# Performance work log

Measured on AMD Instinct MI355X. Metric: run time of the kernel, lower is better.

## Reference

```python
import jax, jax.numpy as jnp
import numpy as np

B, T, F = 128, 1024, 128
H, A, L = 128, 128, 7


def setup_inputs() -> dict:
    key = jax.random.key(0)
    ks = jax.random.split(key, 10)
    s = 0.1  # init scale
    return {
        "x": jax.random.normal(ks[0], (B, T, F), dtype=jnp.float32),
        "Wih": jax.random.normal(ks[1], (L, 4 * H, F), dtype=jnp.float32) * s,
        "Whh": jax.random.normal(ks[2], (L, 4 * H, H), dtype=jnp.float32) * s,
        "bih": jax.random.normal(ks[3], (L, 4 * H), dtype=jnp.float32) * s,
        "bhh": jax.random.normal(ks[4], (L, 4 * H), dtype=jnp.float32) * s,
        "Wa": jax.random.normal(ks[5], (A, H), dtype=jnp.float32) * s,
        "ba": jax.random.normal(ks[6], (A,), dtype=jnp.float32) * s,
        "Wf": jax.random.normal(ks[7], (1, H), dtype=jnp.float32) * s,
        "bf": jax.random.normal(ks[8], (1,), dtype=jnp.float32) * s,
    }


def _lstm_layer(x, Wih_l, Whh_l, bih_l, bhh_l):
    # x: [B, T, F_in] -> hidden sequence [B, T, H]; PyTorch gate order i,f,g,o.
    b, t, _ = x.shape
    xg = jnp.einsum('bti,gi->btg', x, Wih_l) + bih_l + bhh_l  # [B, T, 4H]

    def step(carry, xg_t):
        h, c = carry
        z = xg_t + h @ Whh_l.T  # [B, 4H]
        i, f, g, o = jnp.split(z, 4, axis=-1)
        c = jax.nn.sigmoid(f) * c + jax.nn.sigmoid(i) * jnp.tanh(g)
        h = jax.nn.sigmoid(o) * jnp.tanh(c)
        return (h, c), h

    h0 = jnp.zeros((b, H), x.dtype)
    (_, _), hs = jax.lax.scan(step, (h0, h0), jnp.swapaxes(xg, 0, 1))
    return jnp.swapaxes(hs, 0, 1)  # [B, T, H]


def reference(x, Wih, Whh, bih, bhh, Wa, ba, Wf, bf):
    out = x
    for l in range(Wih.shape[0]):  # fixed small layer count
        out = _lstm_layer(out, Wih[l], Whh[l], bih[l], bhh[l])
    # attention: softmax over time of tanh(Linear(out))  -> [B, T, A]
    attn = jax.nn.softmax(jnp.tanh(jnp.einsum('bth,ah->bta', out, Wa) + ba), axis=1)
    applied = jnp.einsum('bta,bth->bah', attn, out)  # bmm(attn^T, out): [B, A, H]
    logits = applied[:, -1, :] @ Wf.T + bf  # last attention head row -> [B, 1]
    return jax.nn.sigmoid(logits)
```

## Files before the change

kernel.cpp:

```cpp
#include <hip/hip_runtime.h>
#include <cstdint>
#include <cstddef>

#define DEV __device__ __forceinline__

typedef __attribute__((ext_vector_type(4))) float    f32x4;
typedef __attribute__((ext_vector_type(4))) _Float16 f16x4;
typedef __attribute__((ext_vector_type(8))) _Float16 f16x8;

static constexpr int B_ = 128, T_ = 1024, F_ = 128, H_ = 128, L_ = 7;
static constexpr int M_ = B_ * T_;

DEV float fexp2(float x){
#if __has_builtin(__builtin_amdgcn_exp2f)
  return __builtin_amdgcn_exp2f(x);
#else
  return exp2f(x);
#endif
}
DEV float frcp(float x){
#if __has_builtin(__builtin_amdgcn_rcpf)
  return __builtin_amdgcn_rcpf(x);
#else
  return 1.0f/x;
#endif
}
DEV float fsig(float x){ return frcp(1.f + fexp2(-1.44269504f*x)); }
DEV float ftanh(float x){
  x = fminf(10.f, fmaxf(-10.f, x));
  float e = fexp2(2.88539008f*x);
  return (e - 1.f) * frcp(e + 1.f);
}
DEV f16x4 ntld4(const _Float16* p){ return __builtin_nontemporal_load((const f16x4*)p); }
DEV void  ntst4(_Float16* p, f16x4 v){ __builtin_nontemporal_store(v, (f16x4*)p); }
DEV f16x8 ntld8(const _Float16* p){ return __builtin_nontemporal_load((const f16x8*)p); }

__global__ void k_cvt_x(const float4* __restrict__ x4, f16x4* __restrict__ xo, int n4){
  int i = blockIdx.x*blockDim.x + threadIdx.x;
  int stride = gridDim.x*blockDim.x;
  for (; i < n4; i += stride){
    float4 v = x4[i];
    f16x4 o = {(_Float16)v.x, (_Float16)v.y, (_Float16)v.z, (_Float16)v.w};
    xo[i] = o;
  }
}

__global__ void k_cvt_w(const float* __restrict__ Wih, const float* __restrict__ Whh,
                        const float* __restrict__ bih, const float* __restrict__ bhh,
                        _Float16* __restrict__ Wc, float* __restrict__ biasp){
  int idx = blockIdx.x*blockDim.x + threadIdx.x;
  int l    = idx >> 17;
  int rem  = idx & 131071;
  int m    = rem >> 8;
  int k    = rem & 255;
  int gate = m & 3, hrow = m >> 2;
  int srow = l*512 + gate*128 + hrow;
  float v = (k < 128) ? Whh[(size_t)srow*128 + k] : Wih[(size_t)srow*128 + (k-128)];
  Wc[idx] = (_Float16)v;
  if (idx < L_*512){
    int bl = idx >> 9, r = idx & 511;
    int bh = r >> 2, bg = r & 3;
    int s = bl*512 + bg*128 + bh;
    biasp[idx] = bih[s] + bhh[s];
  }
}

__global__ __launch_bounds__(512, 2) void k_recur(
    const _Float16* __restrict__ xcvt,
    _Float16* __restrict__ buf0, _Float16* __restrict__ buf1,
    const _Float16* __restrict__ Wc, const float4* __restrict__ biasp,
    int* __restrict__ flags){
  const int wg = blockIdx.x;
  const int layer = wg >> 3;
  const int g = wg & 7;
  const int tid = threadIdx.x;
  const int w = tid >> 6, l64 = tid & 63;
  const int q = l64 >> 4, i = l64 & 15;

  const _Float16* src = (layer == 0) ? xcvt : (((layer - 1) & 1) ? buf1 : buf0);
  _Float16* dst = (layer & 1) ? buf1 : buf0;

  __shared__ _Float16 hx[2][16][264];

  f16x8 wf[4][8];
  {
    const _Float16* wbase = Wc + ((size_t)layer*512 + i)*256 + 8*q;
#pragma unroll
    for (int mt = 0; mt < 4; ++mt)
#pragma unroll
      for (int kt = 0; kt < 8; ++kt)
        wf[mt][kt] = *(const f16x8*)(wbase + (size_t)(16*(4*w+mt))*256 + 32*kt);
  }
  f32x4 bs[4];
#pragma unroll
  for (int mt = 0; mt < 4; ++mt){
    float4 bv = biasp[layer*128 + 4*(4*w+mt) + q];
    f32x4 t = {bv.x, bv.y, bv.z, bv.w};
    bs[mt] = t;
  }
  float cst[4] = {0.f, 0.f, 0.f, 0.f};

  const int bb = tid >> 5;
  const int cc = tid & 31;
  const size_t srow = ((size_t)(g*16 + bb))*T_*H_;
  const _Float16* xsrc = src + srow + cc*4;
  _Float16*       hdst = dst + srow + cc*4;
  int* fIn  = flags + ((layer - 1)*8 + g)*128;
  int* fOut = flags + (layer*8 + g)*128;

  auto poll = [&](int* p){
    if (tid == 0){
      while (__hip_atomic_load(p, __ATOMIC_RELAXED, __HIP_MEMORY_SCOPE_AGENT) == 0)
        __builtin_amdgcn_s_sleep(2);
    }
    __syncthreads();
  };

  if (layer > 0) poll(fIn + 0);
  {
    f16x4 z4 = {(_Float16)0.f, (_Float16)0.f, (_Float16)0.f, (_Float16)0.f};
    *(f16x4*)&hx[0][bb][cc*4] = z4;
    f16x4 x0 = ntld4(xsrc);
    *(f16x4*)&hx[0][bb][128 + cc*4] = x0;
  }
  f16x4 xn1 = ntld4(xsrc + (size_t)H_);
  __syncthreads();

  for (int t = 0; t < T_; ++t){
    const int cur = t & 1, nxt = cur ^ 1;
    if (layer > 0 && ((t + 2) & 7) == 0 && (t + 2) < T_) poll(fIn + ((t + 2) >> 3));
    int tp = (t + 2 < T_) ? t + 2 : T_ - 1;
    f16x4 xn2 = ntld4(xsrc + (size_t)tp*H_);
    f16x4 freg;
    if (t > 0) freg = *(const f16x4*)&hx[cur][bb][cc*4];
    f16x8 bf[8];
#pragma unroll
    for (int kt = 0; kt < 8; ++kt)
      bf[kt] = *(const f16x8*)&hx[cur][i][32*kt + 8*q];
    f32x4 acc[4];
#pragma unroll
    for (int mt = 0; mt < 4; ++mt){
      acc[mt] = bs[mt];
#pragma unroll
      for (int kt = 0; kt < 8; ++kt)
        acc[mt] = __builtin_amdgcn_mfma_f32_16x16x32_f16(wf[mt][kt], bf[kt], acc[mt], 0, 0, 0);
    }
    if (t > 0) ntst4(hdst + (size_t)(t - 1)*H_, freg);
#pragma unroll
    for (int mt = 0; mt < 4; ++mt){
      f32x4 z = acc[mt];
      cst[mt] = fsig(z[1])*cst[mt] + fsig(z[0])*ftanh(z[2]);
      float h = fsig(z[3])*ftanh(cst[mt]);
      hx[nxt][i][4*(4*w + mt) + q] = (_Float16)h;
    }
    *(f16x4*)&hx[nxt][bb][128 + cc*4] = xn1;
    xn1 = xn2;
    asm volatile("s_waitcnt lgkmcnt(0)\n\ts_barrier" ::: "memory");
    if (layer < 6 && t > 0 && (t & 7) == 0){
      asm volatile("s_waitcnt vmcnt(0)" ::: "memory");
      __syncthreads();
      if (tid == 0)
        (void)__hip_atomic_fetch_add(fOut + ((t >> 3) - 1), 1, __ATOMIC_RELAXED, __HIP_MEMORY_SCOPE_AGENT);
    }
  }
  {
    f16x4 freg = *(const f16x4*)&hx[0][bb][cc*4];
    ntst4(hdst + (size_t)(T_ - 1)*H_, freg);
  }
  if (layer < 6){
    asm volatile("s_waitcnt vmcnt(0)" ::: "memory");
    __syncthreads();
    if (tid == 0)
      (void)__hip_atomic_fetch_add(fOut + 127, 1, __ATOMIC_RELAXED, __HIP_MEMORY_SCOPE_AGENT);
  }
}

__global__ __launch_bounds__(256) void k_attn(const _Float16* __restrict__ out,
                                              const float* __restrict__ Wa, const float* __restrict__ ba,
                                              const float* __restrict__ Wf, const float* __restrict__ bfv,
                                              float* __restrict__ y){
  int b = blockIdx.x, tid = threadIdx.x;
  __shared__ float was[H_];
  __shared__ float p[T_];
  __shared__ float red[64];
  __shared__ float app[256];
  if (tid < H_) was[tid] = Wa[127*H_ + tid];
  __syncthreads();
  float bav = ba[127];
  for (int t = tid; t < T_; t += 256){
    const _Float16* row = out + (size_t)(b*T_ + t)*H_;
    float acc = 0.f;
#pragma unroll
    for (int k = 0; k < H_; k += 8){
      f16x8 u = ntld8(row + k);
      acc += (float)u[0]*was[k+0] + (float)u[1]*was[k+1]
           + (float)u[2]*was[k+2] + (float)u[3]*was[k+3]
           + (float)u[4]*was[k+4] + (float)u[5]*was[k+5]
           + (float)u[6]*was[k+6] + (float)u[7]*was[k+7];
    }
    p[t] = ftanh(acc + bav);
  }
  __syncthreads();
  float m = -1e30f;
  for (int t = tid; t < T_; t += 256) m = fmaxf(m, p[t]);
  for (int off = 32; off; off >>= 1) m = fmaxf(m, __shfl_xor(m, off));
  if ((tid & 63) == 0) red[tid >> 6] = m;
  __syncthreads();
  if (tid == 0) red[8] = fmaxf(fmaxf(red[0], red[1]), fmaxf(red[2], red[3]));
  __syncthreads();
  float smax = red[8];
  float lsum = 0.f;
  for (int t = tid; t < T_; t += 256){
    float e = fexp2(1.44269504f*(p[t] - smax));
    p[t] = e; lsum += e;
  }
  for (int off = 32; off; off >>= 1) lsum += __shfl_xor(lsum, off);
  if ((tid & 63) == 0) red[16 + (tid >> 6)] = lsum;
  __syncthreads();
  float rden = frcp(red[16] + red[17] + red[18] + red[19]);
  int h = tid & (H_ - 1);
  int half = tid >> 7;
  float acc = 0.f;
  for (int t = half*512; t < half*512 + 512; ++t)
    acc += p[t] * (float)__builtin_nontemporal_load(out + (size_t)(b*T_ + t)*H_ + h);
  app[tid] = acc;
  __syncthreads();
  if (tid < H_){
    float applied = (app[tid] + app[tid + H_]) * rden;
    float v = applied * Wf[tid];
    for (int off = 32; off; off >>= 1) v += __shfl_xor(v, off);
    if (tid == 0)  red[32] = v;
    if (tid == 64) red[33] = v;
  }
  __syncthreads();
  if (tid == 0) y[b] = fsig(red[32] + red[33] + bfv[0]);
}

extern "C" void kernel_launch(void* const* d_in, const int* in_sizes, int n_in,
                              void* d_out, int out_size, void* d_ws, size_t ws_size,
                              hipStream_t stream){
  const float* x   = (const float*)d_in[0];
  const float* Wih = (const float*)d_in[1];
  const float* Whh = (const float*)d_in[2];
  const float* bih = (const float*)d_in[3];
  const float* bhh = (const float*)d_in[4];
  const float* Wa  = (const float*)d_in[5];
  const float* ba  = (const float*)d_in[6];
  const float* Wf  = (const float*)d_in[7];
  const float* bfv = (const float*)d_in[8];
  float* y = (float*)d_out;

  char* ws = (char*)d_ws;
  size_t off = 0;
  auto alloc = [&](size_t bytes) -> void* {
    void* p = ws + off; off += (bytes + 255) & ~(size_t)255; return p;
  };
  _Float16* xcvt  = (_Float16*)alloc((size_t)M_*H_*2);
  _Float16* buf0  = (_Float16*)alloc((size_t)M_*H_*2);
  _Float16* buf1  = (_Float16*)alloc((size_t)M_*H_*2);
  _Float16* Wc    = (_Float16*)alloc((size_t)L_*512*256*2);
  float*    biasp = (float*)   alloc((size_t)L_*512*4);
  int*      flags = (int*)     alloc((size_t)6*8*128*4);

  hipMemsetAsync(flags, 0, (size_t)6*8*128*4, stream);
  k_cvt_x<<<2048, 256, 0, stream>>>((const float4*)x, (f16x4*)xcvt, M_*F_/4);
  k_cvt_w<<<3584, 256, 0, stream>>>(Wih, Whh, bih, bhh, Wc, biasp);
  k_recur<<<56, 512, 0, stream>>>(xcvt, buf0, buf1, Wc, (const float4*)biasp, flags);
  k_attn<<<128, 256, 0, stream>>>(buf0, Wa, ba, Wf, bfv, y);
}
```

Baseline: 1.543 ms.

## Split LSTM recurrence across 16 waves with direct-register input operands

The recurrent kernel moves from 8 to 16 waves per workgroup (1024 threads), so each wave holds two gate tiles instead of four and the per-step MFMA chain is half as long. The input-projection operands now come straight from global memory into registers one step ahead, which shrinks the shared h/x buffer to the hidden state only. The weight and bias layout is permuted to match, the loop is unrolled by two, tanh is rewritten in sigmoid form, and the layer flags become plain stores. In exchange it adds more per-step barrier participants and fewer registers per thread, and it depends on the new global loads arriving in time.

```diff
diff --git a/kernel.cpp b/kernel.cpp
--- a/kernel.cpp
+++ b/kernel.cpp
@@ -5,11 +5,13 @@
 #define DEV __device__ __forceinline__
 
 typedef __attribute__((ext_vector_type(4))) float    f32x4;
+typedef __attribute__((ext_vector_type(2))) _Float16 f16x2;
 typedef __attribute__((ext_vector_type(4))) _Float16 f16x4;
 typedef __attribute__((ext_vector_type(8))) _Float16 f16x8;
 
 static constexpr int B_ = 128, T_ = 1024, F_ = 128, H_ = 128, L_ = 7;
 static constexpr int M_ = B_ * T_;
+static constexpr int NCH = 128;
 
 DEV float fexp2(float x){
 #if __has_builtin(__builtin_amdgcn_exp2f)
@@ -26,12 +28,7 @@
 #endif
 }
 DEV float fsig(float x){ return frcp(1.f + fexp2(-1.44269504f*x)); }
-DEV float ftanh(float x){
-  x = fminf(10.f, fmaxf(-10.f, x));
-  float e = fexp2(2.88539008f*x);
-  return (e - 1.f) * frcp(e + 1.f);
-}
-DEV f16x4 ntld4(const _Float16* p){ return __builtin_nontemporal_load((const f16x4*)p); }
+DEV float ftanh(float x){ return 2.f*frcp(1.f + fexp2(-2.88539008f*x)) - 1.f; }
 DEV void  ntst4(_Float16* p, f16x4 v){ __builtin_nontemporal_store(v, (f16x4*)p); }
 DEV f16x8 ntld8(const _Float16* p){ return __builtin_nontemporal_load((const f16x8*)p); }
 
@@ -47,66 +44,70 @@
 
 __global__ void k_cvt_w(const float* __restrict__ Wih, const float* __restrict__ Whh,
                         const float* __restrict__ bih, const float* __restrict__ bhh,
-                        _Float16* __restrict__ Wc, float* __restrict__ biasp){
+                        _Float16* __restrict__ Wc, float* __restrict__ biasc){
   int idx = blockIdx.x*blockDim.x + threadIdx.x;
   int l    = idx >> 17;
   int rem  = idx & 131071;
-  int m    = rem >> 8;
+  int m2   = rem >> 8;
   int k    = rem & 255;
-  int gate = m & 3, hrow = m >> 2;
-  int srow = l*512 + gate*128 + hrow;
+  int W  = m2 >> 5;
+  int mt = (m2 >> 4) & 1;
+  int q  = (m2 >> 2) & 3;
+  int r  = m2 & 3;
+  int hrow = 8*W + 2*q + mt;
+  int srow = l*512 + r*128 + hrow;
   float v = (k < 128) ? Whh[(size_t)srow*128 + k] : Wih[(size_t)srow*128 + (k-128)];
   Wc[idx] = (_Float16)v;
   if (idx < L_*512){
-    int bl = idx >> 9, r = idx & 511;
-    int bh = r >> 2, bg = r & 3;
-    int s = bl*512 + bg*128 + bh;
-    biasp[idx] = bih[s] + bhh[s];
-  }
-}
-
-__global__ __launch_bounds__(512, 2) void k_recur(
+    int bl = idx >> 9, bm = idx & 511;
+    int bW = bm >> 5, bmt = (bm >> 4) & 1, bq = (bm >> 2) & 3, br = bm & 3;
+    int bs = bl*512 + br*128 + (8*bW + 2*bq + bmt);
+    biasc[idx] = bih[bs] + bhh[bs];
+  }
+}
+
+__global__ __launch_bounds__(1024) void k_wave(
     const _Float16* __restrict__ xcvt,
     _Float16* __restrict__ buf0, _Float16* __restrict__ buf1,
-    const _Float16* __restrict__ Wc, const float4* __restrict__ biasp,
+    const _Float16* __restrict__ Wc, const float4* __restrict__ biasc,
     int* __restrict__ flags){
   const int wg = blockIdx.x;
   const int layer = wg >> 3;
   const int g = wg & 7;
   const int tid = threadIdx.x;
-  const int w = tid >> 6, l64 = tid & 63;
-  const int q = l64 >> 4, i = l64 & 15;
+  const int W = tid >> 6;
+  const int q = (tid >> 4) & 3;
+  const int i = tid & 15;
 
   const _Float16* src = (layer == 0) ? xcvt : (((layer - 1) & 1) ? buf1 : buf0);
   _Float16* dst = (layer & 1) ? buf1 : buf0;
 
-  __shared__ _Float16 hx[2][16][264];
-
-  f16x8 wf[4][8];
+  __shared__ _Float16 hx[2][16][132];
+
+  f16x8 wf[2][8];
   {
-    const _Float16* wbase = Wc + ((size_t)layer*512 + i)*256 + 8*q;
+    const _Float16* wbase = Wc + ((size_t)(layer*512) + 32*W + i)*256 + 8*q;
 #pragma unroll
-    for (int mt = 0; mt < 4; ++mt)
+    for (int mt = 0; mt < 2; ++mt)
 #pragma unroll
       for (int kt = 0; kt < 8; ++kt)
-        wf[mt][kt] = *(const f16x8*)(wbase + (size_t)(16*(4*w+mt))*256 + 32*kt);
-  }
-  f32x4 bs[4];
-#pragma unroll
-  for (int mt = 0; mt < 4; ++mt){
-    float4 bv = biasp[layer*128 + 4*(4*w+mt) + q];
-    f32x4 t = {bv.x, bv.y, bv.z, bv.w};
-    bs[mt] = t;
-  }
-  float cst[4] = {0.f, 0.f, 0.f, 0.f};
-
+        wf[mt][kt] = *(const f16x8*)(wbase + (size_t)(16*mt)*256 + 32*kt);
+  }
+  f32x4 bias0, bias1;
+  {
+    float4 b0 = biasc[layer*128 + 8*W + q];
+    float4 b1 = biasc[layer*128 + 8*W + 4 + q];
+    bias0 = f32x4{b0.x, b0.y, b0.z, b0.w};
+    bias1 = f32x4{b1.x, b1.y, b1.z, b1.w};
+  }
+  float c0 = 0.f, c1 = 0.f;
+
+  const _Float16* xbase = src + ((size_t)(g*16 + i))*T_*H_ + 8*q;
   const int bb = tid >> 5;
   const int cc = tid & 31;
-  const size_t srow = ((size_t)(g*16 + bb))*T_*H_;
-  const _Float16* xsrc = src + srow + cc*4;
-  _Float16*       hdst = dst + srow + cc*4;
-  int* fIn  = flags + ((layer - 1)*8 + g)*128;
-  int* fOut = flags + (layer*8 + g)*128;
+  _Float16* hdst = dst + ((size_t)(g*16 + (bb & 15)))*T_*H_ + cc*4;
+  int* fIn  = flags + ((layer > 0 ? layer - 1 : 0)*8 + g)*NCH;
+  int* fOut = flags + (layer*8 + g)*NCH;
 
   auto poll = [&](int* p){
     if (tid == 0){
@@ -117,53 +118,74 @@
   };
 
   if (layer > 0) poll(fIn + 0);
-  {
+  if (tid < 512){
     f16x4 z4 = {(_Float16)0.f, (_Float16)0.f, (_Float16)0.f, (_Float16)0.f};
     *(f16x4*)&hx[0][bb][cc*4] = z4;
-    f16x4 x0 = ntld4(xsrc);
-    *(f16x4*)&hx[0][bb][128 + cc*4] = x0;
-  }
-  f16x4 xn1 = ntld4(xsrc + (size_t)H_);
-  __syncthreads();
-
-  for (int t = 0; t < T_; ++t){
-    const int cur = t & 1, nxt = cur ^ 1;
-    if (layer > 0 && ((t + 2) & 7) == 0 && (t + 2) < T_) poll(fIn + ((t + 2) >> 3));
-    int tp = (t + 2 < T_) ? t + 2 : T_ - 1;
-    f16x4 xn2 = ntld4(xsrc + (size_t)tp*H_);
-    f16x4 freg;
-    if (t > 0) freg = *(const f16x4*)&hx[cur][bb][cc*4];
-    f16x8 bf[8];
-#pragma unroll
-    for (int kt = 0; kt < 8; ++kt)
-      bf[kt] = *(const f16x8*)&hx[cur][i][32*kt + 8*q];
-    f32x4 acc[4];
-#pragma unroll
-    for (int mt = 0; mt < 4; ++mt){
-      acc[mt] = bs[mt];
-#pragma unroll
-      for (int kt = 0; kt < 8; ++kt)
-        acc[mt] = __builtin_amdgcn_mfma_f32_16x16x32_f16(wf[mt][kt], bf[kt], acc[mt], 0, 0, 0);
-    }
-    if (t > 0) ntst4(hdst + (size_t)(t - 1)*H_, freg);
-#pragma unroll
-    for (int mt = 0; mt < 4; ++mt){
-      f32x4 z = acc[mt];
-      cst[mt] = fsig(z[1])*cst[mt] + fsig(z[0])*ftanh(z[2]);
-      float h = fsig(z[3])*ftanh(cst[mt]);
-      hx[nxt][i][4*(4*w + mt) + q] = (_Float16)h;
-    }
-    *(f16x4*)&hx[nxt][bb][128 + cc*4] = xn1;
-    xn1 = xn2;
-    asm volatile("s_waitcnt lgkmcnt(0)\n\ts_barrier" ::: "memory");
+  }
+  f16x8 bx0 = *(const f16x8*)(xbase +  0);
+  f16x8 bx1 = *(const f16x8*)(xbase + 32);
+  f16x8 bx2 = *(const f16x8*)(xbase + 64);
+  f16x8 bx3 = *(const f16x8*)(xbase + 96);
+  __syncthreads();
+
+#define MF(Wf, Bf, Acc) Acc = __builtin_amdgcn_mfma_f32_16x16x32_f16(Wf, Bf, Acc, 0, 0, 0)
+
+#define BODY(CUR, TT)                                                            \
+  {                                                                              \
+    f16x4 freg = {};                                                             \
+    if ((TT) > 0 && tid < 512) freg = *(const f16x4*)&hx[CUR][bb][cc*4];         \
+    f32x4 a0 = bias0, a1 = bias1;                                                \
+                           \
+    MF(wf[0][4], bx0, a0); MF(wf[1][4], bx0, a1);                                \
+    MF(wf[0][5], bx1, a0); MF(wf[1][5], bx1, a1);                                \
+    MF(wf[0][6], bx2, a0); MF(wf[1][6], bx2, a1);                                \
+    MF(wf[0][7], bx3, a0); MF(wf[1][7], bx3, a1);                                \
+                                                         \
+    f16x8 bf0 = *(const f16x8*)&hx[CUR][i][ 0 + 8*q];                            \
+    f16x8 bf1 = *(const f16x8*)&hx[CUR][i][32 + 8*q];                            \
+    f16x8 bf2 = *(const f16x8*)&hx[CUR][i][64 + 8*q];                            \
+    f16x8 bf3 = *(const f16x8*)&hx[CUR][i][96 + 8*q];                            \
+         \
+    { int rp = (TT) + 1; if (rp > T_ - 1) rp = T_ - 1;                           \
+      const _Float16* xr = xbase + (size_t)rp*H_;                                \
+      bx0 = *(const f16x8*)(xr +  0);                                            \
+      bx1 = *(const f16x8*)(xr + 32);                                            \
+      bx2 = *(const f16x8*)(xr + 64);                                            \
+      bx3 = *(const f16x8*)(xr + 96); }                                          \
+                                                                     \
+    MF(wf[0][0], bf0, a0); MF(wf[1][0], bf0, a1);                                \
+    MF(wf[0][1], bf1, a0); MF(wf[1][1], bf1, a1);                                \
+    MF(wf[0][2], bf2, a0); MF(wf[1][2], bf2, a1);                                \
+    MF(wf[0][3], bf3, a0); MF(wf[1][3], bf3, a1);                                \
+    if ((TT) > 0 && tid < 512) ntst4(hdst + (size_t)((TT) - 1)*H_, freg);        \
+                           \
+    float h0, h1;                                                                \
+    { float si = fsig(a0[0]), sf = fsig(a0[1]);                                  \
+      float gt = ftanh(a0[2]), so = fsig(a0[3]);                                 \
+      c0 = sf*c0 + si*gt; h0 = so*ftanh(c0); }                                   \
+    { float si = fsig(a1[0]), sf = fsig(a1[1]);                                  \
+      float gt = ftanh(a1[2]), so = fsig(a1[3]);                                 \
+      c1 = sf*c1 + si*gt; h1 = so*ftanh(c1); }                                   \
+    f16x2 hv = {(_Float16)h0, (_Float16)h1};                                     \
+    *(f16x2*)&hx[(CUR) ^ 1][i][8*W + 2*q] = hv;                                  \
+    asm volatile("s_waitcnt lgkmcnt(0)\n\ts_barrier" ::: "memory");              \
+  }
+
+  for (int t = 0; t < T_; t += 2){
+    BODY(0, t)
     if (layer < 6 && t > 0 && (t & 7) == 0){
       asm volatile("s_waitcnt vmcnt(0)" ::: "memory");
       __syncthreads();
       if (tid == 0)
-        (void)__hip_atomic_fetch_add(fOut + ((t >> 3) - 1), 1, __ATOMIC_RELAXED, __HIP_MEMORY_SCOPE_AGENT);
+        __hip_atomic_store(fOut + ((t >> 3) - 1), 1, __ATOMIC_RELAXED, __HIP_MEMORY_SCOPE_AGENT);
     }
-  }
-  {
+    if (layer > 0 && ((t + 2) & 7) == 0 && (t + 2) < T_) poll(fIn + ((t + 2) >> 3));
+    BODY(1, t + 1)
+  }
+#undef BODY
+#undef MF
+
+  if (tid < 512){
     f16x4 freg = *(const f16x4*)&hx[0][bb][cc*4];
     ntst4(hdst + (size_t)(T_ - 1)*H_, freg);
   }
@@ -171,7 +193,7 @@
     asm volatile("s_waitcnt vmcnt(0)" ::: "memory");
     __syncthreads();
     if (tid == 0)
-      (void)__hip_atomic_fetch_add(fOut + 127, 1, __ATOMIC_RELAXED, __HIP_MEMORY_SCOPE_AGENT);
+      __hip_atomic_store(fOut + (NCH - 1), 1, __ATOMIC_RELAXED, __HIP_MEMORY_SCOPE_AGENT);
   }
 }
 
@@ -259,12 +281,12 @@
   _Float16* buf0  = (_Float16*)alloc((size_t)M_*H_*2);
   _Float16* buf1  = (_Float16*)alloc((size_t)M_*H_*2);
   _Float16* Wc    = (_Float16*)alloc((size_t)L_*512*256*2);
-  float*    biasp = (float*)   alloc((size_t)L_*512*4);
-  int*      flags = (int*)     alloc((size_t)6*8*128*4);
-
-  hipMemsetAsync(flags, 0, (size_t)6*8*128*4, stream);
+  float*    biasc = (float*)   alloc((size_t)L_*512*4);
+  int*      flags = (int*)     alloc((size_t)L_*8*NCH*4);
+
+  hipMemsetAsync(flags, 0, (size_t)L_*8*NCH*4, stream);
   k_cvt_x<<<2048, 256, 0, stream>>>((const float4*)x, (f16x4*)xcvt, M_*F_/4);
-  k_cvt_w<<<3584, 256, 0, stream>>>(Wih, Whh, bih, bhh, Wc, biasp);
-  k_recur<<<56, 512, 0, stream>>>(xcvt, buf0, buf1, Wc, (const float4*)biasp, flags);
+  k_cvt_w<<<3584, 256, 0, stream>>>(Wih, Whh, bih, bhh, Wc, biasc);
+  k_wave<<<56, 1024, 0, stream>>>(xcvt, buf0, buf1, Wc, (const float4*)biasc, flags);
   k_attn<<<128, 256, 0, stream>>>(buf0, Wa, ba, Wf, bfv, y);
 }
```

After: 2.347 ms. +52.1%, slower.

## Split input projection into producer workgroups feeding recurrent workgroups via ring buffer

Applied to the files above, without the earlier changes.

Adds 56 producer workgroups that compute the input-to-hidden gate projections for 8-timestep chunks into a ring buffer in global memory, with flag-based handshakes. The recurrent workgroups then run only the hidden-to-hidden MFMAs (K=128 instead of 256) and load precomputed gates ahead of time, which halves the serial critical-path matrix work. It also simplifies tanh, unrolls the timestep loop by two, and relaxes the launch bound. The cost is extra global traffic, more flag polling, and the risk that producer throughput or the ring-buffer backpressure becomes the new bottleneck.

```diff
diff --git a/kernel.cpp b/kernel.cpp
--- a/kernel.cpp
+++ b/kernel.cpp
@@ -10,6 +10,9 @@
 
 static constexpr int B_ = 128, T_ = 1024, F_ = 128, H_ = 128, L_ = 7;
 static constexpr int M_ = B_ * T_;
+static constexpr int NCH  = 128;
+static constexpr int RING = 8;
+static constexpr int ROWE = 128*16*4;
 
 DEV float fexp2(float x){
 #if __has_builtin(__builtin_amdgcn_exp2f)
@@ -26,14 +29,18 @@
 #endif
 }
 DEV float fsig(float x){ return frcp(1.f + fexp2(-1.44269504f*x)); }
-DEV float ftanh(float x){
-  x = fminf(10.f, fmaxf(-10.f, x));
-  float e = fexp2(2.88539008f*x);
-  return (e - 1.f) * frcp(e + 1.f);
-}
+DEV float ftanh(float x){ return 2.f*frcp(1.f + fexp2(-2.88539008f*x)) - 1.f; }
+DEV void  ntst4(_Float16* p, f16x4 v){ __builtin_nontemporal_store(v, (f16x4*)p); }
 DEV f16x4 ntld4(const _Float16* p){ return __builtin_nontemporal_load((const f16x4*)p); }
-DEV void  ntst4(_Float16* p, f16x4 v){ __builtin_nontemporal_store(v, (f16x4*)p); }
 DEV f16x8 ntld8(const _Float16* p){ return __builtin_nontemporal_load((const f16x8*)p); }
+
+DEV void poll_flag(int* p, int tid){
+  if (tid == 0){
+    while (__hip_atomic_load(p, __ATOMIC_RELAXED, __HIP_MEMORY_SCOPE_AGENT) == 0)
+      __builtin_amdgcn_s_sleep(2);
+  }
+  __syncthreads();
+}
 
 __global__ void k_cvt_x(const float4* __restrict__ x4, f16x4* __restrict__ xo, int n4){
   int i = blockIdx.x*blockDim.x + threadIdx.x;
@@ -47,133 +54,204 @@
 
 __global__ void k_cvt_w(const float* __restrict__ Wih, const float* __restrict__ Whh,
                         const float* __restrict__ bih, const float* __restrict__ bhh,
-                        _Float16* __restrict__ Wc, float* __restrict__ biasp){
+                        _Float16* __restrict__ WhhC, _Float16* __restrict__ WihC,
+                        float* __restrict__ biasc){
   int idx = blockIdx.x*blockDim.x + threadIdx.x;
-  int l    = idx >> 17;
-  int rem  = idx & 131071;
-  int m    = rem >> 8;
-  int k    = rem & 255;
-  int gate = m & 3, hrow = m >> 2;
-  int srow = l*512 + gate*128 + hrow;
-  float v = (k < 128) ? Whh[(size_t)srow*128 + k] : Wih[(size_t)srow*128 + (k-128)];
-  Wc[idx] = (_Float16)v;
+  int l   = idx >> 16;
+  int rem = idx & 65535;
+  int m2  = rem >> 7;
+  int k   = rem & 127;
+  int W = m2 >> 6, mt = (m2 >> 4) & 3, q = (m2 >> 2) & 3, r = m2 & 3;
+  int hrow = 16*W + 4*q + mt;
+  int srow = l*512 + r*128 + hrow;
+  WhhC[idx] = (_Float16)Whh[(size_t)srow*128 + k];
+  WihC[idx] = (_Float16)Wih[(size_t)srow*128 + k];
   if (idx < L_*512){
-    int bl = idx >> 9, r = idx & 511;
-    int bh = r >> 2, bg = r & 3;
-    int s = bl*512 + bg*128 + bh;
-    biasp[idx] = bih[s] + bhh[s];
-  }
-}
-
-__global__ __launch_bounds__(512, 2) void k_recur(
+    int bl = idx >> 9, bm = idx & 511;
+    int bW = bm >> 6, bmt = (bm >> 4) & 3, bq = (bm >> 2) & 3, br = bm & 3;
+    int bs = bl*512 + br*128 + (16*bW + 4*bq + bmt);
+    biasc[idx] = bih[bs] + bhh[bs];
+  }
+}
+
+#define MF(Wf, Bf, Acc) Acc = __builtin_amdgcn_mfma_f32_16x16x32_f16(Wf, Bf, Acc, 0, 0, 0)
+
+__global__ __launch_bounds__(512) void k_fused(
     const _Float16* __restrict__ xcvt,
     _Float16* __restrict__ buf0, _Float16* __restrict__ buf1,
-    const _Float16* __restrict__ Wc, const float4* __restrict__ biasp,
-    int* __restrict__ flags){
-  const int wg = blockIdx.x;
-  const int layer = wg >> 3;
-  const int g = wg & 7;
+    const _Float16* __restrict__ WhhC, const _Float16* __restrict__ WihC,
+    const float4* __restrict__ biascF4,
+    _Float16* __restrict__ xz, int* __restrict__ flags){
+  const int wg  = blockIdx.x;
   const int tid = threadIdx.x;
-  const int w = tid >> 6, l64 = tid & 63;
-  const int q = l64 >> 4, i = l64 & 15;
-
-  const _Float16* src = (layer == 0) ? xcvt : (((layer - 1) & 1) ? buf1 : buf0);
-  _Float16* dst = (layer & 1) ? buf1 : buf0;
-
-  __shared__ _Float16 hx[2][16][264];
-
-  f16x8 wf[4][8];
-  {
-    const _Float16* wbase = Wc + ((size_t)layer*512 + i)*256 + 8*q;
-#pragma unroll
-    for (int mt = 0; mt < 4; ++mt)
-#pragma unroll
-      for (int kt = 0; kt < 8; ++kt)
-        wf[mt][kt] = *(const f16x8*)(wbase + (size_t)(16*(4*w+mt))*256 + 32*kt);
-  }
-  f32x4 bs[4];
-#pragma unroll
-  for (int mt = 0; mt < 4; ++mt){
-    float4 bv = biasp[layer*128 + 4*(4*w+mt) + q];
-    f32x4 t = {bv.x, bv.y, bv.z, bv.w};
-    bs[mt] = t;
-  }
-  float cst[4] = {0.f, 0.f, 0.f, 0.f};
-
-  const int bb = tid >> 5;
-  const int cc = tid & 31;
-  const size_t srow = ((size_t)(g*16 + bb))*T_*H_;
-  const _Float16* xsrc = src + srow + cc*4;
-  _Float16*       hdst = dst + srow + cc*4;
-  int* fIn  = flags + ((layer - 1)*8 + g)*128;
-  int* fOut = flags + (layer*8 + g)*128;
-
-  auto poll = [&](int* p){
-    if (tid == 0){
-      while (__hip_atomic_load(p, __ATOMIC_RELAXED, __HIP_MEMORY_SCOPE_AGENT) == 0)
-        __builtin_amdgcn_s_sleep(2);
+  const int W  = tid >> 6;
+  const int lq = (tid >> 4) & 3;
+  const int li = tid & 15;
+
+  __shared__ _Float16 smem[128*132];
+
+  int* recF = flags;
+  int* xzF  = flags + 7*8*NCH;
+
+  if (wg < 56){
+    const int layer = wg >> 3, g = wg & 7;
+    _Float16* dst = (layer & 1) ? buf1 : buf0;
+    _Float16 (*hx)[16][132] = (_Float16(*)[16][132])smem;
+
+    f16x8 wfH[4][4];
+    {
+      const _Float16* wb = WhhC + ((size_t)(layer*512) + 64*W + li)*128 + 8*lq;
+#pragma unroll
+      for (int mt = 0; mt < 4; ++mt)
+#pragma unroll
+        for (int kt = 0; kt < 4; ++kt)
+          wfH[mt][kt] = *(const f16x8*)(wb + (size_t)(16*mt)*128 + 32*kt);
+    }
+    float c0_ = 0.f, c1_ = 0.f, c2_ = 0.f, c3_ = 0.f;
+
+    const int bb = tid >> 5, cc = tid & 31;
+    _Float16* hdst = dst + ((size_t)(g*16 + bb))*T_*H_ + cc*4;
+    const _Float16* xzg = xz + ((size_t)(layer*8 + g))*RING*8*ROWE;
+    int* xzFl = xzF + (layer*8 + g)*NCH;
+    int* myF  = recF + (layer*8 + g)*NCH;
+    const int xzoff = ((16*W + 4*lq)*16 + li)*4;
+
+    poll_flag(xzFl + 0, tid);
+    {
+      f16x4 z4 = {(_Float16)0.f, (_Float16)0.f, (_Float16)0.f, (_Float16)0.f};
+      *(f16x4*)&hx[0][bb][cc*4] = z4;
+    }
+    f16x4 xzA[4], xzB[4];
+#pragma unroll
+    for (int mt = 0; mt < 4; ++mt){
+      xzA[mt] = ntld4(xzg + xzoff + mt*64);
+      xzB[mt] = ntld4(xzg + (size_t)ROWE + xzoff + mt*64);
     }
     __syncthreads();
-  };
-
-  if (layer > 0) poll(fIn + 0);
-  {
-    f16x4 z4 = {(_Float16)0.f, (_Float16)0.f, (_Float16)0.f, (_Float16)0.f};
-    *(f16x4*)&hx[0][bb][cc*4] = z4;
-    f16x4 x0 = ntld4(xsrc);
-    *(f16x4*)&hx[0][bb][128 + cc*4] = x0;
-  }
-  f16x4 xn1 = ntld4(xsrc + (size_t)H_);
-  __syncthreads();
-
-  for (int t = 0; t < T_; ++t){
-    const int cur = t & 1, nxt = cur ^ 1;
-    if (layer > 0 && ((t + 2) & 7) == 0 && (t + 2) < T_) poll(fIn + ((t + 2) >> 3));
-    int tp = (t + 2 < T_) ? t + 2 : T_ - 1;
-    f16x4 xn2 = ntld4(xsrc + (size_t)tp*H_);
-    f16x4 freg;
-    if (t > 0) freg = *(const f16x4*)&hx[cur][bb][cc*4];
-    f16x8 bf[8];
-#pragma unroll
-    for (int kt = 0; kt < 8; ++kt)
-      bf[kt] = *(const f16x8*)&hx[cur][i][32*kt + 8*q];
-    f32x4 acc[4];
-#pragma unroll
-    for (int mt = 0; mt < 4; ++mt){
-      acc[mt] = bs[mt];
-#pragma unroll
-      for (int kt = 0; kt < 8; ++kt)
-        acc[mt] = __builtin_amdgcn_mfma_f32_16x16x32_f16(wf[mt][kt], bf[kt], acc[mt], 0, 0, 0);
-    }
-    if (t > 0) ntst4(hdst + (size_t)(t - 1)*H_, freg);
-#pragma unroll
-    for (int mt = 0; mt < 4; ++mt){
-      f32x4 z = acc[mt];
-      cst[mt] = fsig(z[1])*cst[mt] + fsig(z[0])*ftanh(z[2]);
-      float h = fsig(z[3])*ftanh(cst[mt]);
-      hx[nxt][i][4*(4*w + mt) + q] = (_Float16)h;
-    }
-    *(f16x4*)&hx[nxt][bb][128 + cc*4] = xn1;
-    xn1 = xn2;
-    asm volatile("s_waitcnt lgkmcnt(0)\n\ts_barrier" ::: "memory");
-    if (layer < 6 && t > 0 && (t & 7) == 0){
+
+#define RBODY(CUR, TT, XZ)                                                      \
+  {                                                                             \
+    f16x4 freg = {};                                                            \
+    if ((TT) > 0) freg = *(const f16x4*)&hx[CUR][bb][cc*4];                     \
+    f32x4 a0 = {(float)XZ[0][0], (float)XZ[0][1], (float)XZ[0][2], (float)XZ[0][3]}; \
+    f32x4 a1 = {(float)XZ[1][0], (float)XZ[1][1], (float)XZ[1][2], (float)XZ[1][3]}; \
+    f32x4 a2 = {(float)XZ[2][0], (float)XZ[2][1], (float)XZ[2][2], (float)XZ[2][3]}; \
+    f32x4 a3 = {(float)XZ[3][0], (float)XZ[3][1], (float)XZ[3][2], (float)XZ[3][3]}; \
+    f16x8 bf0 = *(const f16x8*)&hx[CUR][li][ 0 + 8*lq];                         \
+    f16x8 bf1 = *(const f16x8*)&hx[CUR][li][32 + 8*lq];                         \
+    f16x8 bf2 = *(const f16x8*)&hx[CUR][li][64 + 8*lq];                         \
+    f16x8 bf3 = *(const f16x8*)&hx[CUR][li][96 + 8*lq];                         \
+    { int rp = (TT) + 2; if (rp > T_ - 1) rp = T_ - 1;                          \
+      const _Float16* xr = xzg + (size_t)(rp & 63)*ROWE + xzoff;                \
+      XZ[0] = ntld4(xr); XZ[1] = ntld4(xr + 64);                                \
+      XZ[2] = ntld4(xr + 128); XZ[3] = ntld4(xr + 192); }                       \
+    MF(wfH[0][0], bf0, a0); MF(wfH[1][0], bf0, a1);                             \
+    MF(wfH[2][0], bf0, a2); MF(wfH[3][0], bf0, a3);                             \
+    MF(wfH[0][1], bf1, a0); MF(wfH[1][1], bf1, a1);                             \
+    MF(wfH[2][1], bf1, a2); MF(wfH[3][1], bf1, a3);                             \
+    MF(wfH[0][2], bf2, a0); MF(wfH[1][2], bf2, a1);                             \
+    MF(wfH[2][2], bf2, a2); MF(wfH[3][2], bf2, a3);                             \
+    MF(wfH[0][3], bf3, a0); MF(wfH[1][3], bf3, a1);                             \
+    MF(wfH[2][3], bf3, a2); MF(wfH[3][3], bf3, a3);                             \
+    if ((TT) > 0) ntst4(hdst + (size_t)((TT) - 1)*H_, freg);                    \
+    f16x4 hv;                                                                   \
+    { float si = fsig(a0[0]), sf = fsig(a0[1]);                                 \
+      float gt = ftanh(a0[2]), so = fsig(a0[3]);                                \
+      c0_ = sf*c0_ + si*gt; hv[0] = (_Float16)(so*ftanh(c0_)); }                \
+    { float si = fsig(a1[0]), sf = fsig(a1[1]);                                 \
+      float gt = ftanh(a1[2]), so = fsig(a1[3]);                                \
+      c1_ = sf*c1_ + si*gt; hv[1] = (_Float16)(so*ftanh(c1_)); }                \
+    { float si = fsig(a2[0]), sf = fsig(a2[1]);                                 \
+      float gt = ftanh(a2[2]), so = fsig(a2[3]);                                \
+      c2_ = sf*c2_ + si*gt; hv[2] = (_Float16)(so*ftanh(c2_)); }                \
+    { float si = fsig(a3[0]), sf = fsig(a3[1]);                                 \
+      float gt = ftanh(a3[2]), so = fsig(a3[3]);                                \
+      c3_ = sf*c3_ + si*gt; hv[3] = (_Float16)(so*ftanh(c3_)); }                \
+    *(f16x4*)&hx[(CUR) ^ 1][li][16*W + 4*lq] = hv;                              \
+    asm volatile("s_waitcnt lgkmcnt(0)\n\ts_barrier" ::: "memory");             \
+  }
+
+    for (int t = 0; t < T_; t += 2){
+      if ((t & 7) == 6) poll_flag(xzFl + ((t + 2) >> 3), tid);
+      RBODY(0, t, xzA)
+      if (t > 0 && (t & 7) == 0){
+        asm volatile("s_waitcnt vmcnt(0)" ::: "memory");
+        __syncthreads();
+        if (tid == 0)
+          __hip_atomic_store(myF + ((t >> 3) - 1), 1, __ATOMIC_RELAXED, __HIP_MEMORY_SCOPE_AGENT);
+      }
+      RBODY(1, t + 1, xzB)
+    }
+#undef RBODY
+    {
+      f16x4 freg = *(const f16x4*)&hx[0][bb][cc*4];
+      ntst4(hdst + (size_t)(T_ - 1)*H_, freg);
+    }
+    asm volatile("s_waitcnt vmcnt(0)" ::: "memory");
+    __syncthreads();
+    if (tid == 0)
+      __hip_atomic_store(myF + (NCH - 1), 1, __ATOMIC_RELAXED, __HIP_MEMORY_SCOPE_AGENT);
+
+  } else {
+    const int wg2 = wg - 56;
+    const int layer = wg2 >> 3, g = wg2 & 7;
+    const _Float16* hsrc = (layer == 0) ? xcvt : (((layer - 1) & 1) ? buf1 : buf0);
+    _Float16 (*hb)[132] = (_Float16(*)[132])smem;
+    _Float16* xzw = xz + ((size_t)(layer*8 + g))*RING*8*ROWE;
+    int* xzFl = xzF + (layer*8 + g)*NCH;
+    int* inF  = recF + ((layer > 0 ? layer - 1 : 0)*8 + g)*NCH;
+    int* selfF = recF + (layer*8 + g)*NCH;
+
+    const int n  = tid >> 2;
+    const int qd = tid & 3;
+    const int st = n >> 4, sb = n & 15;
+    const _Float16* srcp = hsrc + ((size_t)(g*16 + sb))*T_*H_ + (size_t)st*H_ + qd*32;
+
+    for (int c = 0; c < NCH; ++c){
+      if (layer > 0) poll_flag(inF + c, tid);
+      if (c >= RING) poll_flag(selfF + (c - RING), tid);
+      {
+        const _Float16* sp = srcp + (size_t)(8*c)*H_;
+        f16x8 v0 = ntld8(sp), v1 = ntld8(sp + 8), v2 = ntld8(sp + 16), v3 = ntld8(sp + 24);
+        *(f16x8*)&hb[n][qd*32 +  0] = v0;
+        *(f16x8*)&hb[n][qd*32 +  8] = v1;
+        *(f16x8*)&hb[n][qd*32 + 16] = v2;
+        *(f16x8*)&hb[n][qd*32 + 24] = v3;
+      }
+      __syncthreads();
+#pragma unroll
+      for (int j = 0; j < 4; ++j){
+        const int m0 = 64*W + 16*j;
+        f16x8 A0, A1, A2, A3;
+        {
+          const _Float16* ab = WihC + ((size_t)(layer*512 + m0 + li))*128 + 8*lq;
+          A0 = *(const f16x8*)(ab);      A1 = *(const f16x8*)(ab + 32);
+          A2 = *(const f16x8*)(ab + 64); A3 = *(const f16x8*)(ab + 96);
+        }
+        float4 bv = biascF4[layer*128 + 16*W + 4*j + lq];
+        f32x4 bias = {bv.x, bv.y, bv.z, bv.w};
+        const int hrow = 16*W + 4*lq + j;
+#pragma unroll
+        for (int nt = 0; nt < 8; ++nt){
+          f16x8 B0 = *(const f16x8*)&hb[nt*16 + li][ 0 + 8*lq];
+          f16x8 B1 = *(const f16x8*)&hb[nt*16 + li][32 + 8*lq];
+          f16x8 B2 = *(const f16x8*)&hb[nt*16 + li][64 + 8*lq];
+          f16x8 B3 = *(const f16x8*)&hb[nt*16 + li][96 + 8*lq];
+          f32x4 acc = bias;
+          MF(A0, B0, acc); MF(A1, B1, acc); MF(A2, B2, acc); MF(A3, B3, acc);
+          int row = c*8 + nt;
+          f16x4 o = {(_Float16)acc[0], (_Float16)acc[1], (_Float16)acc[2], (_Float16)acc[3]};
+          ntst4(xzw + (size_t)(row & 63)*ROWE + (size_t)(hrow*16 + li)*4, o);
+        }
+      }
       asm volatile("s_waitcnt vmcnt(0)" ::: "memory");
       __syncthreads();
       if (tid == 0)
-        (void)__hip_atomic_fetch_add(fOut + ((t >> 3) - 1), 1, __ATOMIC_RELAXED, __HIP_MEMORY_SCOPE_AGENT);
-    }
-  }
-  {
-    f16x4 freg = *(const f16x4*)&hx[0][bb][cc*4];
-    ntst4(hdst + (size_t)(T_ - 1)*H_, freg);
-  }
-  if (layer < 6){
-    asm volatile("s_waitcnt vmcnt(0)" ::: "memory");
-    __syncthreads();
-    if (tid == 0)
-      (void)__hip_atomic_fetch_add(fOut + 127, 1, __ATOMIC_RELAXED, __HIP_MEMORY_SCOPE_AGENT);
-  }
-}
+        __hip_atomic_store(xzFl + c, 1, __ATOMIC_RELAXED, __HIP_MEMORY_SCOPE_AGENT);
+    }
+  }
+}
+#undef MF
 
 __global__ __launch_bounds__(256) void k_attn(const _Float16* __restrict__ out,
                                               const float* __restrict__ Wa, const float* __restrict__ ba,
@@ -258,13 +336,16 @@
   _Float16* xcvt  = (_Float16*)alloc((size_t)M_*H_*2);
   _Float16* buf0  = (_Float16*)alloc((size_t)M_*H_*2);
   _Float16* buf1  = (_Float16*)alloc((size_t)M_*H_*2);
-  _Float16* Wc    = (_Float16*)alloc((size_t)L_*512*256*2);
-  float*    biasp = (float*)   alloc((size_t)L_*512*4);
-  int*      flags = (int*)     alloc((size_t)6*8*128*4);
-
-  hipMemsetAsync(flags, 0, (size_t)6*8*128*4, stream);
+  _Float16* WhhC  = (_Float16*)alloc((size_t)L_*512*128*2);
+  _Float16* WihC  = (_Float16*)alloc((size_t)L_*512*128*2);
+  float*    biasc = (float*)   alloc((size_t)L_*512*4);
+  _Float16* xzbuf = (_Float16*)alloc((size_t)56*RING*8*ROWE*2);
+  int*      flags = (int*)     alloc((size_t)2*7*8*NCH*4);
+
+  hipMemsetAsync(flags, 0, (size_t)2*7*8*NCH*4, stream);
   k_cvt_x<<<2048, 256, 0, stream>>>((const float4*)x, (f16x4*)xcvt, M_*F_/4);
-  k_cvt_w<<<3584, 256, 0, stream>>>(Wih, Whh, bih, bhh, Wc, biasp);
-  k_recur<<<56, 512, 0, stream>>>(xcvt, buf0, buf1, Wc, (const float4*)biasp, flags);
+  k_cvt_w<<<1792, 256, 0, stream>>>(Wih, Whh, bih, bhh, WhhC, WihC, biasc);
+  k_fused<<<112, 512, 0, stream>>>(xcvt, buf0, buf1, WhhC, WihC,
+                                   (const float4*)biasc, xzbuf, flags);
   k_attn<<<128, 256, 0, stream>>>(buf0, Wa, ba, Wf, bfv, y);
 }
```

New measurement: 4.558 ms. +195.4%, slower.

## Split recurrent step into two half-K MFMA phases overlapped across wave groups

Applied to the files above, without the earlier changes.

Restructures the LSTM recurrence kernel so waves 0-3 and 4-7 each own a different half of the K dimension per phase. One group computes its first-half MFMAs while the other finishes the previous step's second half and gate math, aiming to hide gate latency behind matrix work on the serial time dependence. The weight layout is permuted so each wave owns full gate rows, and the x input moves to a triple-buffered shared staging area with deeper prefetch. Tanh is rewritten as a sigmoid form and flag signalling changes from atomic add to store. This adds a second barrier per step and trickier buffer indexing.

```diff
diff --git a/kernel.cpp b/kernel.cpp
--- a/kernel.cpp
+++ b/kernel.cpp
@@ -10,6 +10,7 @@
 
 static constexpr int B_ = 128, T_ = 1024, F_ = 128, H_ = 128, L_ = 7;
 static constexpr int M_ = B_ * T_;
+static constexpr int NCH = 128;
 
 DEV float fexp2(float x){
 #if __has_builtin(__builtin_amdgcn_exp2f)
@@ -26,12 +27,7 @@
 #endif
 }
 DEV float fsig(float x){ return frcp(1.f + fexp2(-1.44269504f*x)); }
-DEV float ftanh(float x){
-  x = fminf(10.f, fmaxf(-10.f, x));
-  float e = fexp2(2.88539008f*x);
-  return (e - 1.f) * frcp(e + 1.f);
-}
-DEV f16x4 ntld4(const _Float16* p){ return __builtin_nontemporal_load((const f16x4*)p); }
+DEV float ftanh(float x){ return 2.f*frcp(1.f + fexp2(-2.88539008f*x)) - 1.f; }
 DEV void  ntst4(_Float16* p, f16x4 v){ __builtin_nontemporal_store(v, (f16x4*)p); }
 DEV f16x8 ntld8(const _Float16* p){ return __builtin_nontemporal_load((const f16x8*)p); }
 
@@ -47,68 +43,71 @@
 
 __global__ void k_cvt_w(const float* __restrict__ Wih, const float* __restrict__ Whh,
                         const float* __restrict__ bih, const float* __restrict__ bhh,
-                        _Float16* __restrict__ Wc, float* __restrict__ biasp){
+                        _Float16* __restrict__ Wc, float* __restrict__ biasc){
   int idx = blockIdx.x*blockDim.x + threadIdx.x;
   int l    = idx >> 17;
   int rem  = idx & 131071;
-  int m    = rem >> 8;
+  int m2   = rem >> 8;
   int k    = rem & 255;
-  int gate = m & 3, hrow = m >> 2;
-  int srow = l*512 + gate*128 + hrow;
+  int W = m2 >> 6, mt = (m2 >> 4) & 3, q = (m2 >> 2) & 3, r = m2 & 3;
+  int hrow = 16*W + 4*q + mt;
+  int srow = l*512 + r*128 + hrow;
   float v = (k < 128) ? Whh[(size_t)srow*128 + k] : Wih[(size_t)srow*128 + (k-128)];
   Wc[idx] = (_Float16)v;
   if (idx < L_*512){
-    int bl = idx >> 9, r = idx & 511;
-    int bh = r >> 2, bg = r & 3;
-    int s = bl*512 + bg*128 + bh;
-    biasp[idx] = bih[s] + bhh[s];
-  }
-}
-
-__global__ __launch_bounds__(512, 2) void k_recur(
+    int bl = idx >> 9, bm = idx & 511;
+    int bW = bm >> 6, bmt = (bm >> 4) & 3, bq = (bm >> 2) & 3, br = bm & 3;
+    int bs = bl*512 + br*128 + (16*bW + 4*bq + bmt);
+    biasc[idx] = bih[bs] + bhh[bs];
+  }
+}
+
+#define MF(Wf, Bf, Acc) Acc = __builtin_amdgcn_mfma_f32_16x16x32_f16(Wf, Bf, Acc, 0, 0, 0)
+
+__global__ __launch_bounds__(512, 2) void k_wave(
     const _Float16* __restrict__ xcvt,
     _Float16* __restrict__ buf0, _Float16* __restrict__ buf1,
-    const _Float16* __restrict__ Wc, const float4* __restrict__ biasp,
+    const _Float16* __restrict__ Wc, const float4* __restrict__ biascF4,
     int* __restrict__ flags){
   const int wg = blockIdx.x;
-  const int layer = wg >> 3;
-  const int g = wg & 7;
+  const int layer = wg >> 3, g = wg & 7;
   const int tid = threadIdx.x;
-  const int w = tid >> 6, l64 = tid & 63;
-  const int q = l64 >> 4, i = l64 & 15;
+  const int W = tid >> 6;
+  const bool E = (W < 4);
+  const int q = (tid >> 4) & 3;
+  const int i = tid & 15;
 
   const _Float16* src = (layer == 0) ? xcvt : (((layer - 1) & 1) ? buf1 : buf0);
   _Float16* dst = (layer & 1) ? buf1 : buf0;
 
-  __shared__ _Float16 hx[2][16][264];
+  __shared__ _Float16 hx[2][16][132];
+  __shared__ _Float16 xb[3][16][132];
 
   f16x8 wf[4][8];
   {
-    const _Float16* wbase = Wc + ((size_t)layer*512 + i)*256 + 8*q;
+    const _Float16* wb = Wc + ((size_t)(layer*512) + 64*W + i)*256 + 8*q;
 #pragma unroll
     for (int mt = 0; mt < 4; ++mt)
 #pragma unroll
       for (int kt = 0; kt < 8; ++kt)
-        wf[mt][kt] = *(const f16x8*)(wbase + (size_t)(16*(4*w+mt))*256 + 32*kt);
+        wf[mt][kt] = *(const f16x8*)(wb + (size_t)(16*mt)*256 + 32*kt);
   }
   f32x4 bs[4];
 #pragma unroll
   for (int mt = 0; mt < 4; ++mt){
-    float4 bv = biasp[layer*128 + 4*(4*w+mt) + q];
-    f32x4 t = {bv.x, bv.y, bv.z, bv.w};
-    bs[mt] = t;
+    float4 bv = biascF4[layer*128 + 16*W + 4*mt + q];
+    bs[mt] = f32x4{bv.x, bv.y, bv.z, bv.w};
   }
   float cst[4] = {0.f, 0.f, 0.f, 0.f};
-
-  const int bb = tid >> 5;
-  const int cc = tid & 31;
-  const size_t srow = ((size_t)(g*16 + bb))*T_*H_;
-  const _Float16* xsrc = src + srow + cc*4;
-  _Float16*       hdst = dst + srow + cc*4;
-  int* fIn  = flags + ((layer - 1)*8 + g)*128;
-  int* fOut = flags + (layer*8 + g)*128;
-
-  auto poll = [&](int* p){
+  f32x4 acc[4];
+
+  const int bb = tid >> 5, cc = tid & 31;
+  const _Float16* xsrc = src + ((size_t)(g*16 + bb))*T_*H_ + cc*4;
+  _Float16*       hdst = dst + ((size_t)(g*16 + bb))*T_*H_ + cc*4;
+  int* fIn  = flags + ((layer > 0 ? layer - 1 : 0)*8 + g)*NCH;
+  int* fOut = flags + (layer*8 + g)*NCH;
+
+  auto pollf = [&](int* p){
     if (tid == 0){
       while (__hip_atomic_load(p, __ATOMIC_RELAXED, __HIP_MEMORY_SCOPE_AGENT) == 0)
         __builtin_amdgcn_s_sleep(2);
@@ -116,64 +115,106 @@
     __syncthreads();
   };
 
-  if (layer > 0) poll(fIn + 0);
+#define MF4(KT, B) { MF(wf[0][KT], B, acc[0]); MF(wf[1][KT], B, acc[1]); \
+                     MF(wf[2][KT], B, acc[2]); MF(wf[3][KT], B, acc[3]); }
+
+  auto mfma_half1 = [&](int ph, int xs){
+    f16x8 b0 = *(const f16x8*)&hx[ph][i][ 0 + 8*q];
+    f16x8 b1 = *(const f16x8*)&hx[ph][i][32 + 8*q];
+    f16x8 x0 = *(const f16x8*)&xb[xs][i][ 0 + 8*q];
+    f16x8 x1 = *(const f16x8*)&xb[xs][i][32 + 8*q];
+#pragma unroll
+    for (int mt = 0; mt < 4; ++mt) acc[mt] = bs[mt];
+    MF4(0, b0) MF4(1, b1) MF4(4, x0) MF4(5, x1)
+  };
+  auto mfma_half2 = [&](int ph, int xs){
+    f16x8 b2 = *(const f16x8*)&hx[ph][i][64 + 8*q];
+    f16x8 b3 = *(const f16x8*)&hx[ph][i][96 + 8*q];
+    f16x8 x2 = *(const f16x8*)&xb[xs][i][64 + 8*q];
+    f16x8 x3 = *(const f16x8*)&xb[xs][i][96 + 8*q];
+    MF4(2, b2) MF4(3, b3) MF4(6, x2) MF4(7, x3)
+  };
+  auto gates_write = [&](int pd){
+    f16x4 hv;
+#pragma unroll
+    for (int mt = 0; mt < 4; ++mt){
+      f32x4 z = acc[mt];
+      float si = fsig(z[0]), sf = fsig(z[1]);
+      float gt = ftanh(z[2]), so = fsig(z[3]);
+      cst[mt] = sf*cst[mt] + si*gt;
+      hv[mt] = (_Float16)(so*ftanh(cst[mt]));
+    }
+    *(f16x4*)&hx[pd][i][16*W + 4*q] = hv;
+  };
+
+  if (layer > 0) pollf(fIn + 0);
   {
     f16x4 z4 = {(_Float16)0.f, (_Float16)0.f, (_Float16)0.f, (_Float16)0.f};
-    *(f16x4*)&hx[0][bb][cc*4] = z4;
-    f16x4 x0 = ntld4(xsrc);
-    *(f16x4*)&hx[0][bb][128 + cc*4] = x0;
-  }
-  f16x4 xn1 = ntld4(xsrc + (size_t)H_);
-  __syncthreads();
-
+    *(f16x4*)&hx[1][bb][cc*4] = z4;
+    f16x4 r0 = *(const f16x4*)(xsrc);
+    f16x4 r1 = *(const f16x4*)(xsrc + (size_t)H_);
+    *(f16x4*)&xb[0][bb][cc*4] = r0;
+    *(f16x4*)&xb[1][bb][cc*4] = r1;
+  }
+  f16x4 xn0 = *(const f16x4*)(xsrc + (size_t)2*H_);
+  f16x4 xn1 = *(const f16x4*)(xsrc + (size_t)3*H_);
+  __syncthreads();
+
+  int sCur = 0;
+  int sStg = 2;
   for (int t = 0; t < T_; ++t){
-    const int cur = t & 1, nxt = cur ^ 1;
-    if (layer > 0 && ((t + 2) & 7) == 0 && (t + 2) < T_) poll(fIn + ((t + 2) >> 3));
-    int tp = (t + 2 < T_) ? t + 2 : T_ - 1;
-    f16x4 xn2 = ntld4(xsrc + (size_t)tp*H_);
-    f16x4 freg;
-    if (t > 0) freg = *(const f16x4*)&hx[cur][bb][cc*4];
-    f16x8 bf[8];
-#pragma unroll
-    for (int kt = 0; kt < 8; ++kt)
-      bf[kt] = *(const f16x8*)&hx[cur][i][32*kt + 8*q];
-    f32x4 acc[4];
-#pragma unroll
-    for (int mt = 0; mt < 4; ++mt){
-      acc[mt] = bs[mt];
-#pragma unroll
-      for (int kt = 0; kt < 8; ++kt)
-        acc[mt] = __builtin_amdgcn_mfma_f32_16x16x32_f16(wf[mt][kt], bf[kt], acc[mt], 0, 0, 0);
-    }
-    if (t > 0) ntst4(hdst + (size_t)(t - 1)*H_, freg);
-#pragma unroll
-    for (int mt = 0; mt < 4; ++mt){
-      f32x4 z = acc[mt];
-      cst[mt] = fsig(z[1])*cst[mt] + fsig(z[0])*ftanh(z[2]);
-      float h = fsig(z[3])*ftanh(cst[mt]);
-      hx[nxt][i][4*(4*w + mt) + q] = (_Float16)h;
-    }
-    *(f16x4*)&hx[nxt][bb][128 + cc*4] = xn1;
-    xn1 = xn2;
+    const int pr = (t + 1) & 1;
+    const int pw = t & 1;
+    if (E){
+      mfma_half1(pr, sCur);
+    } else if (t > 0){
+      mfma_half2(pw, sStg);
+      gates_write(pr);
+    }
     asm volatile("s_waitcnt lgkmcnt(0)\n\ts_barrier" ::: "memory");
-    if (layer < 6 && t > 0 && (t & 7) == 0){
+    if (E){
+      mfma_half2(pr, sCur);
+      gates_write(pw);
+    } else {
+      mfma_half1(pr, sCur);
+    }
+    if (t > 0){
+      f16x4 freg = *(const f16x4*)&hx[pr][bb][cc*4];
+      ntst4(hdst + (size_t)(t - 1)*H_, freg);
+    }
+    *(f16x4*)&xb[sStg][bb][cc*4] = xn0;
+    xn0 = xn1;
+    if (layer > 0 && ((t + 4) & 7) == 0 && (t + 4) < T_) pollf(fIn + ((t + 4) >> 3));
+    { int rp = (t + 4 < T_) ? t + 4 : T_ - 1;
+      xn1 = *(const f16x4*)(xsrc + (size_t)rp*H_); }
+    asm volatile("s_waitcnt lgkmcnt(0)\n\ts_barrier" ::: "memory");
+    if (t > 0 && (t & 7) == 0){
       asm volatile("s_waitcnt vmcnt(0)" ::: "memory");
       __syncthreads();
       if (tid == 0)
-        (void)__hip_atomic_fetch_add(fOut + ((t >> 3) - 1), 1, __ATOMIC_RELAXED, __HIP_MEMORY_SCOPE_AGENT);
-    }
+        __hip_atomic_store(fOut + ((t >> 3) - 1), 1, __ATOMIC_RELAXED, __HIP_MEMORY_SCOPE_AGENT);
+    }
+    sCur = (sCur == 2) ? 0 : sCur + 1;
+    sStg = (sStg == 2) ? 0 : sStg + 1;
   }
   {
-    f16x4 freg = *(const f16x4*)&hx[0][bb][cc*4];
+    const int pr = (T_ + 1) & 1;
+    const int pw = T_ & 1;
+    if (!E){
+      mfma_half2(pw, sStg);
+      gates_write(pr);
+    }
+    asm volatile("s_waitcnt lgkmcnt(0)\n\ts_barrier" ::: "memory");
+    f16x4 freg = *(const f16x4*)&hx[pr][bb][cc*4];
     ntst4(hdst + (size_t)(T_ - 1)*H_, freg);
   }
-  if (layer < 6){
-    asm volatile("s_waitcnt vmcnt(0)" ::: "memory");
-    __syncthreads();
-    if (tid == 0)
-      (void)__hip_atomic_fetch_add(fOut + 127, 1, __ATOMIC_RELAXED, __HIP_MEMORY_SCOPE_AGENT);
-  }
-}
+  asm volatile("s_waitcnt vmcnt(0)" ::: "memory");
+  __syncthreads();
+  if (tid == 0)
+    __hip_atomic_store(fOut + (NCH - 1), 1, __ATOMIC_RELAXED, __HIP_MEMORY_SCOPE_AGENT);
+}
+#undef MF4
+#undef MF
 
 __global__ __launch_bounds__(256) void k_attn(const _Float16* __restrict__ out,
                                               const float* __restrict__ Wa, const float* __restrict__ ba,
@@ -259,12 +300,12 @@
   _Float16* buf0  = (_Float16*)alloc((size_t)M_*H_*2);
   _Float16* buf1  = (_Float16*)alloc((size_t)M_*H_*2);
   _Float16* Wc    = (_Float16*)alloc((size_t)L_*512*256*2);
-  float*    biasp = (float*)   alloc((size_t)L_*512*4);
-  int*      flags = (int*)     alloc((size_t)6*8*128*4);
-
-  hipMemsetAsync(flags, 0, (size_t)6*8*128*4, stream);
+  float*    biasc = (float*)   alloc((size_t)L_*512*4);
+  int*      flags = (int*)     alloc((size_t)L_*8*NCH*4);
+
+  hipMemsetAsync(flags, 0, (size_t)L_*8*NCH*4, stream);
   k_cvt_x<<<2048, 256, 0, stream>>>((const float4*)x, (f16x4*)xcvt, M_*F_/4);
-  k_cvt_w<<<3584, 256, 0, stream>>>(Wih, Whh, bih, bhh, Wc, biasp);
-  k_recur<<<56, 512, 0, stream>>>(xcvt, buf0, buf1, Wc, (const float4*)biasp, flags);
+  k_cvt_w<<<3584, 256, 0, stream>>>(Wih, Whh, bih, bhh, Wc, biasc);
+  k_wave<<<56, 512, 0, stream>>>(xcvt, buf0, buf1, Wc, (const float4*)biasc, flags);
   k_attn<<<128, 256, 0, stream>>>(buf0, Wa, ba, Wf, bfv, y);
 }
```

New measurement: 1.862 ms. 20.7% more time.
